# Kernel tuning notes

Measured on AMD Instinct MI355X. Metric: run time of the kernel, lower is better.

Reference implementation:

```python
import jax, jax.numpy as jnp
import numpy as np
from jax import lax

B, N, C = 8, 1024, 768
H, D = 12, 64
K = 3  # conv kernel size


def dwconv_over_batch(x, w, b):
    """Faithful port of SpatialDepthWisePerHeadConvolution as used in this module.
    x: [B, N, H, D]. The original code treats dim0 (B) as the conv length axis.
    w: [H*D, 1, K] depthwise kernel, b: [H*D].
    Returns [B, N, H, D].
    """
    b_, n_, h_, d_ = x.shape
    xc = jnp.transpose(x, (1, 2, 3, 0)).reshape(n_, h_ * d_, b_)  # [N, HD, B]
    y = lax.conv_general_dilated(
        xc, w, window_strides=(1,), padding=[(K - 1, K - 1)],
        feature_group_count=h_ * d_, dimension_numbers=("NCH", "OIH", "NCH"))
    y = y[:, :, :b_] + b[None, :, None]  # causal slice (drop last K-1)
    return jnp.transpose(y.reshape(n_, h_, d_, b_), (3, 0, 1, 2))


def setup_inputs() -> dict:
    key = jax.random.key(0)
    ks = jax.random.split(key, 12)
    s = 0.02
    inp = {
        "x": jax.random.normal(ks[0], (B, N, C), jnp.float32),
        "wq": jax.random.normal(ks[1], (C, H * D), jnp.float32) * s,
        "wk": jax.random.normal(ks[2], (C, H * D), jnp.float32) * s,
        "wv": jax.random.normal(ks[3], (C, H * D), jnp.float32) * s,
        "bv": jnp.zeros((H * D,), jnp.float32),
        "cq_w": jax.random.normal(ks[4], (H * D, 1, K), jnp.float32) * s,
        "cq_b": jnp.zeros((H * D,), jnp.float32),
        "ck_w": jax.random.normal(ks[5], (H * D, 1, K), jnp.float32) * s,
        "ck_b": jnp.zeros((H * D,), jnp.float32),
        "cv_w": jax.random.normal(ks[6], (H * D, 1, K), jnp.float32) * s,
        "cv_b": jnp.zeros((H * D,), jnp.float32),
        "wo": jax.random.normal(ks[7], (C, C), jnp.float32) * s,
        "bo": jnp.zeros((C,), jnp.float32),
    }
    return inp


def reference(x, wq, wk, wv, bv, cq_w, cq_b, ck_w, ck_b, cv_w, cv_b, wo, bo):
    scale = (C // H) ** -0.5
    # linear -> [B,N,H,D]
    q = (x @ wq).reshape(B, N, H, D)
    k = (x @ wk).reshape(B, N, H, D)
    v = ((x @ wv) + bv).reshape(B, N, H, D)
    # per-head depthwise causal conv (over batch axis, as in the original code)
    q = dwconv_over_batch(q, cq_w, cq_b)
    k = dwconv_over_batch(k, ck_w, ck_b)
    v = dwconv_over_batch(v, cv_w, cv_b)
    # [B,H,N,D]
    q = jnp.transpose(q, (0, 2, 1, 3))
    k = jnp.transpose(k, (0, 2, 1, 3))
    v = jnp.transpose(v, (0, 2, 1, 3))
    scores = jnp.einsum("bhnd,bhmd->bhnm", q, k) * scale
    attn = jax.nn.softmax(scores, axis=-1)
    out = jnp.einsum("bhnm,bhmd->bhnd", attn, v)
    out = jnp.transpose(out, (0, 2, 1, 3)).reshape(B, N, C)
    return out @ wo + bo
```

## Files before the change

kernel.cpp:

```cpp
#include <hip/hip_runtime.h>
#include <math.h>

static constexpr int B_ = 8, N_ = 1024, C_ = 768, H_ = 12, D_ = 64;

typedef __bf16 bf16_t;
typedef bf16_t bf16x8 __attribute__((ext_vector_type(8)));
typedef bf16_t bf16x4 __attribute__((ext_vector_type(4)));
typedef short short4v __attribute__((ext_vector_type(4)));
typedef float f32x4 __attribute__((ext_vector_type(4)));

#define MFMA32(a, b, c) __builtin_amdgcn_mfma_f32_16x16x32_bf16((a), (b), (c), 0, 0, 0)
#define MFMA16(a, b, c) __builtin_amdgcn_mfma_f32_16x16x16bf16_1k( \
    __builtin_bit_cast(short4v, (a)), __builtin_bit_cast(short4v, (b)), (c), 0, 0, 0)

__device__ __forceinline__ unsigned short f2bf(float f) {
    unsigned u = __builtin_bit_cast(unsigned, f);
    u += 0x7FFFu + ((u >> 16) & 1u);
    return (unsigned short)(u >> 16);
}

__device__ __forceinline__ float bf2f(unsigned short u) {
    return __builtin_bit_cast(float, (unsigned)u << 16);
}

__device__ __forceinline__ void gload16(void* lds, const void* g) {
    __builtin_amdgcn_global_load_lds(
        (const __attribute__((address_space(1))) unsigned int*)g,
        (__attribute__((address_space(3))) unsigned int*)lds, 16, 0, 0);
}

__device__ __forceinline__ int swz(int row, int kslot) {
    return row * 128 + (((kslot ^ row) & 7) << 4);
}

__global__ __launch_bounds__(256)
void castx_kernel(const float* __restrict__ in, unsigned short* __restrict__ out)
{
    const int i = blockIdx.x * 256 + threadIdx.x;
    const float4 a = ((const float4*)in)[2 * i];
    const float4 b = ((const float4*)in)[2 * i + 1];
    uint4 o;
    o.x = f2bf(a.x) | ((unsigned)f2bf(a.y) << 16);
    o.y = f2bf(a.z) | ((unsigned)f2bf(a.w) << 16);
    o.z = f2bf(b.x) | ((unsigned)f2bf(b.y) << 16);
    o.w = f2bf(b.z) | ((unsigned)f2bf(b.w) << 16);
    ((uint4*)out)[i] = o;
}

__global__ __launch_bounds__(256)
void castwT4_kernel(const float* w0, const float* w1, const float* w2, const float* w3,
                    unsigned short* o0, unsigned short* o1,
                    unsigned short* o2, unsigned short* o3)
{
    const float* w; unsigned short* wT;
    switch (blockIdx.z) {
        case 0:  w = w0; wT = o0; break;
        case 1:  w = w1; wT = o1; break;
        case 2:  w = w2; wT = o2; break;
        default: w = w3; wT = o3; break;
    }
    __shared__ float T[64][65];
    const int t = threadIdx.x;
    const int k0 = blockIdx.x * 64, n0 = blockIdx.y * 64;
    const int r = t >> 2, c0 = (t & 3) * 16;
#pragma unroll
    for (int j4 = 0; j4 < 4; ++j4) {
        const float4 v = *(const float4*)(w + (size_t)(k0 + r) * 768 + n0 + c0 + j4 * 4);
        T[r][c0 + j4 * 4 + 0] = v.x; T[r][c0 + j4 * 4 + 1] = v.y;
        T[r][c0 + j4 * 4 + 2] = v.z; T[r][c0 + j4 * 4 + 3] = v.w;
    }
    __syncthreads();
    const int nn = t >> 2;
    unsigned short o[16];
#pragma unroll
    for (int j = 0; j < 16; ++j) o[j] = f2bf(T[c0 + j][nn]);
    uint4* dst = (uint4*)(wT + (size_t)(n0 + nn) * 768 + k0 + c0);
    dst[0] = *(uint4*)(o); dst[1] = *(uint4*)(o + 8);
}

template <typename OutT>
__device__ __forceinline__ void gemm_body(const unsigned short* __restrict__ A,
                                          const unsigned short* __restrict__ BT,
                                          const float* __restrict__ bias,
                                          OutT* __restrict__ Cmat,
                                          int Ncols, int Kdim, int row0, int col0)
{
    __shared__ char As[128 * 128];
    __shared__ char Bs[128 * 128];

    const int tid = threadIdx.x, lane = tid & 63, w = tid >> 6;
    const int wr = w >> 1, wc = w & 1;
    const int slot = lane & 7, rsub = lane >> 3;

    f32x4 acc[4][4] = {};

    for (int k0 = 0; k0 < Kdim; k0 += 64) {
#pragma unroll
        for (int c = 0; c < 4; ++c) {
            const int chunk = c * 4 + w;
            const int r = chunk * 8 + rsub;
            gload16(As + chunk * 1024, A + (size_t)(row0 + r) * Kdim + k0 + 8 * (slot ^ (r & 7)));
            gload16(Bs + chunk * 1024, BT + (size_t)(col0 + r) * Kdim + k0 + 8 * (slot ^ (r & 7)));
        }
        __syncthreads();

#pragma unroll
        for (int kk = 0; kk < 2; ++kk) {
            const int kslot = kk * 4 + (lane >> 4);
            bf16x8 af[4], bf[4];
#pragma unroll
            for (int mi = 0; mi < 4; ++mi)
                af[mi] = *(const bf16x8*)(As + swz(wr * 64 + mi * 16 + (lane & 15), kslot));
#pragma unroll
            for (int ni = 0; ni < 4; ++ni)
                bf[ni] = *(const bf16x8*)(Bs + swz(wc * 64 + ni * 16 + (lane & 15), kslot));
#pragma unroll
            for (int mi = 0; mi < 4; ++mi)
#pragma unroll
                for (int ni = 0; ni < 4; ++ni)
                    acc[mi][ni] = MFMA32(af[mi], bf[ni], acc[mi][ni]);
        }
        __syncthreads();
    }

#pragma unroll
    for (int mi = 0; mi < 4; ++mi) {
        const int row = row0 + wr * 64 + mi * 16 + ((lane >> 4) << 2);
#pragma unroll
        for (int ni = 0; ni < 4; ++ni) {
            const int col = col0 + wc * 64 + ni * 16 + (lane & 15);
            const float bv_ = bias ? bias[col] : 0.f;
#pragma unroll
            for (int r = 0; r < 4; ++r) {
                const float v = acc[mi][ni][r] + bv_;
                if constexpr (sizeof(OutT) == 2)
                    Cmat[(size_t)(row + r) * Ncols + col] = (OutT)f2bf(v);
                else
                    Cmat[(size_t)(row + r) * Ncols + col] = v;
            }
        }
    }
}

__global__ __launch_bounds__(256)
void gemm_qkv(const unsigned short* __restrict__ xb,
              const unsigned short* __restrict__ wqT, const unsigned short* __restrict__ wkT,
              const unsigned short* __restrict__ wvT, const float* __restrict__ bv,
              unsigned short* __restrict__ q_lin, unsigned short* __restrict__ k_lin,
              unsigned short* __restrict__ v_lin)
{
    const int by = blockIdx.y, sel = by / 6, colt = by % 6;
    const unsigned short* BT; unsigned short* dst; const float* bias = nullptr;
    if (sel == 0)      { BT = wqT; dst = q_lin; }
    else if (sel == 1) { BT = wkT; dst = k_lin; }
    else               { BT = wvT; dst = v_lin; bias = bv; }
    gemm_body<unsigned short>(xb, BT, bias, dst, C_, C_, blockIdx.x * 128, colt * 128);
}

__global__ __launch_bounds__(256)
void gemm_proj(const unsigned short* __restrict__ A, const unsigned short* __restrict__ BT,
               const float* __restrict__ bias, float* __restrict__ Cmat)
{
    gemm_body<float>(A, BT, bias, Cmat, C_, C_, blockIdx.x * 128, blockIdx.y * 128);
}

__global__ __launch_bounds__(256)
void dwconv_qk(const unsigned short* __restrict__ qlin, const unsigned short* __restrict__ klin,
               const float* __restrict__ cq_w, const float* __restrict__ cq_b,
               const float* __restrict__ ck_w, const float* __restrict__ ck_b,
               unsigned short* __restrict__ qc, unsigned short* __restrict__ kc)
{
    const unsigned short* lin; const float* w; const float* bias;
    unsigned short* out;
    if (blockIdx.y == 0) { lin = qlin; w = cq_w; bias = cq_b; out = qc; }
    else                 { lin = klin; w = ck_w; bias = ck_b; out = kc; }

    const int i = blockIdx.x * 256 + threadIdx.x;
    const int c8 = i % (C_ / 8);
    const int n  = (i / (C_ / 8)) % N_;
    const int b  = i / ((C_ / 8) * N_);
    const int c  = c8 * 8;

    const uint4 z4 = make_uint4(0, 0, 0, 0);
    const uint4 x0 = (b >= 2) ? *(const uint4*)(lin + ((size_t)(b - 2) * N_ + n) * C_ + c) : z4;
    const uint4 x1 = (b >= 1) ? *(const uint4*)(lin + ((size_t)(b - 1) * N_ + n) * C_ + c) : z4;
    const uint4 x2 = *(const uint4*)(lin + ((size_t)b * N_ + n) * C_ + c);
    const unsigned short* u0 = (const unsigned short*)&x0;
    const unsigned short* u1 = (const unsigned short*)&x1;
    const unsigned short* u2 = (const unsigned short*)&x2;

    unsigned short y[8];
#pragma unroll
    for (int j = 0; j < 8; ++j) {
        const float v = w[(c + j) * 3 + 0] * bf2f(u0[j]) +
                        w[(c + j) * 3 + 1] * bf2f(u1[j]) +
                        w[(c + j) * 3 + 2] * bf2f(u2[j]) + bias[c + j];
        y[j] = f2bf(v);
    }
    const int h = c8 >> 3, d0 = (c8 & 7) * 8;
    *(uint4*)(out + (((size_t)b * H_ + h) * N_ + n) * 64 + d0) = *(uint4*)y;
}

__global__ __launch_bounds__(256)
void conv_v_transpose(const unsigned short* __restrict__ vlin, const float* __restrict__ w,
                      const float* __restrict__ bias, unsigned short* __restrict__ vt)
{
    __shared__ unsigned short T[64][72];
    const int t = threadIdx.x;
    const int n0 = blockIdx.x * 64, bh = blockIdx.y;
    const int b = bh / H_, h = bh % H_;
    const int r = t >> 2, c0 = (t & 3) * 16;
    const int cbase = h * 64 + c0;

    float acc[16];
#pragma unroll
    for (int i = 0; i < 16; ++i) acc[i] = bias[cbase + i];
#pragma unroll
    for (int j = 0; j < 3; ++j) {
        const int bb = b - 2 + j;
        if (bb < 0) continue;
        const unsigned short* src = vlin + ((size_t)bb * N_ + n0 + r) * C_ + cbase;
        const uint4 va = *(const uint4*)src;
        const uint4 vb2 = *(const uint4*)(src + 8);
        const unsigned short* u = (const unsigned short*)&va;
        const unsigned short* u2 = (const unsigned short*)&vb2;
#pragma unroll
        for (int i = 0; i < 8; ++i)  acc[i]     += w[(cbase + i) * 3 + j] * bf2f(u[i]);
#pragma unroll
        for (int i = 0; i < 8; ++i)  acc[8 + i] += w[(cbase + 8 + i) * 3 + j] * bf2f(u2[i]);
    }
    unsigned short tmp[16];
#pragma unroll
    for (int i = 0; i < 16; ++i) tmp[i] = f2bf(acc[i]);
    *(uint4*)&T[r][c0] = *(uint4*)tmp;
    *(uint4*)&T[r][c0 + 8] = *(uint4*)(tmp + 8);
    __syncthreads();

    const int d = t >> 2;
    unsigned short o[16];
#pragma unroll
    for (int i = 0; i < 16; ++i) o[i] = T[c0 + i][d];
    uint4* dst = (uint4*)(vt + ((size_t)bh * 64 + d) * N_ + n0 + c0);
    dst[0] = *(uint4*)o; dst[1] = *(uint4*)(o + 8);
}

__global__ __launch_bounds__(256)
void attn_mfma(const unsigned short* __restrict__ Qg, const unsigned short* __restrict__ Kg,
               const unsigned short* __restrict__ Vtg, unsigned short* __restrict__ Og)
{
    __shared__ char Kb[2][8192];
    __shared__ char Vb[2][8192];

    const int tid = threadIdx.x, lane = tid & 63, w = tid >> 6;
    const int g = lane >> 4, q = lane & 15;
    const int slot = lane & 7, rsub = lane >> 3;

    const int id = blockIdx.x;
    const int bh = (id & 7) * 12 + ((id >> 3) % 12);
    const int q0 = (id / 96) * 128;
    const int b = bh / H_, h = bh % H_;

    const unsigned short* Qp = Qg + (size_t)bh * N_ * 64;
    const unsigned short* Kp = Kg + (size_t)bh * N_ * 64;
    const unsigned short* Vp = Vtg + (size_t)bh * 64 * N_;

    bf16x8 qf[2][2];
#pragma unroll
    for (int mi = 0; mi < 2; ++mi)
#pragma unroll
        for (int kk = 0; kk < 2; ++kk)
            qf[mi][kk] = *(const bf16x8*)(Qp + (size_t)(q0 + w * 32 + mi * 16 + q) * 64 + kk * 32 + g * 8);

#pragma unroll
    for (int c = 0; c < 2; ++c) {
        const int chunk = c * 4 + w, r = chunk * 8 + rsub;
        gload16(Kb[0] + chunk * 1024, Kp + (size_t)r * 64 + 8 * (slot ^ (r & 7)));
        gload16(Vb[0] + chunk * 1024, Vp + (size_t)r * N_ + 8 * (slot ^ (r & 7)));
    }
    __syncthreads();

    f32x4 o[2][4] = {};
    float mrun[2] = {0.f, 0.f}, lrun[2] = {0.f, 0.f};
    const float cs = 0.18033688011112042f;

    int buf = 0;
    for (int kt = 0; kt < N_ / 64; ++kt) {
        if (kt < N_ / 64 - 1) {
            const int nb = buf ^ 1;
#pragma unroll
            for (int c = 0; c < 2; ++c) {
                const int chunk = c * 4 + w, r = chunk * 8 + rsub;
                gload16(Kb[nb] + chunk * 1024, Kp + (size_t)((kt + 1) * 64 + r) * 64 + 8 * (slot ^ (r & 7)));
                gload16(Vb[nb] + chunk * 1024, Vp + (size_t)r * N_ + (kt + 1) * 64 + 8 * (slot ^ (r & 7)));
            }
        }

        f32x4 s[2][4] = {};
#pragma unroll
        for (int kk = 0; kk < 2; ++kk) {
            const int kslot = kk * 4 + g;
            bf16x8 kf[4];
#pragma unroll
            for (int ni = 0; ni < 4; ++ni)
                kf[ni] = *(const bf16x8*)(Kb[buf] + swz(ni * 16 + q, kslot));
#pragma unroll
            for (int mi = 0; mi < 2; ++mi)
#pragma unroll
                for (int ni = 0; ni < 4; ++ni)
                    s[mi][ni] = MFMA32(kf[ni], qf[mi][kk], s[mi][ni]);
        }

        bf16x4 pf[2][4];
#pragma unroll
        for (int mi = 0; mi < 2; ++mi) {
            float t[4][4];
#pragma unroll
            for (int ni = 0; ni < 4; ++ni)
#pragma unroll
                for (int rg = 0; rg < 4; ++rg) t[ni][rg] = s[mi][ni][rg] * cs;
            float m0 = t[0][0];
#pragma unroll
            for (int ni = 0; ni < 4; ++ni)
#pragma unroll
                for (int rg = 0; rg < 4; ++rg) m0 = fmaxf(m0, t[ni][rg]);
            m0 = fmaxf(m0, __shfl_xor(m0, 16));
            m0 = fmaxf(m0, __shfl_xor(m0, 32));
            if (__any(m0 > mrun[mi] + 8.f)) {
                const float mnew = fmaxf(mrun[mi], m0);
                const float f = exp2f(mrun[mi] - mnew);
                lrun[mi] *= f;
#pragma unroll
                for (int nd = 0; nd < 4; ++nd) o[mi][nd] *= f;
                mrun[mi] = mnew;
            }
            float sum = 0.f;
#pragma unroll
            for (int ni = 0; ni < 4; ++ni) {
                const float p0 = exp2f(t[ni][0] - mrun[mi]);
                const float p1 = exp2f(t[ni][1] - mrun[mi]);
                const float p2 = exp2f(t[ni][2] - mrun[mi]);
                const float p3 = exp2f(t[ni][3] - mrun[mi]);
                sum += (p0 + p1) + (p2 + p3);
                bf16x4 pk;
                pk[0] = (bf16_t)p0; pk[1] = (bf16_t)p1; pk[2] = (bf16_t)p2; pk[3] = (bf16_t)p3;
                pf[mi][ni] = pk;
            }
            sum += __shfl_xor(sum, 16);
            sum += __shfl_xor(sum, 32);
            lrun[mi] += sum;
        }

#pragma unroll
        for (int ni = 0; ni < 4; ++ni) {
            bf16x4 vf[4];
#pragma unroll
            for (int nd = 0; nd < 4; ++nd) {
                const int d = nd * 16 + q;
                vf[nd] = *(const bf16x4*)(Vb[buf] + d * 128 +
                          ((((2 * ni + (g >> 1)) ^ (d & 7))) << 4) + 8 * (g & 1));
            }
#pragma unroll
            for (int mi = 0; mi < 2; ++mi)
#pragma unroll
                for (int nd = 0; nd < 4; ++nd)
                    o[mi][nd] = MFMA16(vf[nd], pf[mi][ni], o[mi][nd]);
        }

        __syncthreads();
        buf ^= 1;
    }

#pragma unroll
    for (int mi = 0; mi < 2; ++mi) {
        const float inv = 1.0f / lrun[mi];
        const int qrow = q0 + w * 32 + mi * 16 + q;
        unsigned short* orow = Og + ((size_t)b * N_ + qrow) * C_ + h * D_;
#pragma unroll
        for (int nd = 0; nd < 4; ++nd) {
            unsigned short pk[4];
#pragma unroll
            for (int rg = 0; rg < 4; ++rg) pk[rg] = f2bf(o[mi][nd][rg] * inv);
            *(uint2*)(orow + nd * 16 + 4 * g) = *(uint2*)pk;
        }
    }
}

extern "C" void kernel_launch(void* const* d_in, const int* in_sizes, int n_in,
                              void* d_out, int out_size, void* d_ws, size_t ws_size,
                              hipStream_t stream)
{
    (void)in_sizes; (void)n_in; (void)out_size; (void)ws_size;
    const float* x    = (const float*)d_in[0];
    const float* wq   = (const float*)d_in[1];
    const float* wk   = (const float*)d_in[2];
    const float* wv   = (const float*)d_in[3];
    const float* bv   = (const float*)d_in[4];
    const float* cq_w = (const float*)d_in[5];
    const float* cq_b = (const float*)d_in[6];
    const float* ck_w = (const float*)d_in[7];
    const float* ck_b = (const float*)d_in[8];
    const float* cv_w = (const float*)d_in[9];
    const float* cv_b = (const float*)d_in[10];
    const float* wo   = (const float*)d_in[11];
    const float* bo   = (const float*)d_in[12];
    float* out = (float*)d_out;

    char* wsb = (char*)d_ws;
    const size_t T  = (size_t)B_ * N_ * C_;
    const size_t WB = (size_t)2 * 589824;
    unsigned short* xb  = (unsigned short*)wsb;
    unsigned short* wqT = (unsigned short*)(wsb + 2 * T);
    unsigned short* wkT = wqT + 589824;
    unsigned short* wvT = wkT + 589824;
    unsigned short* woT = wvT + 589824;
    char* p = wsb + 2 * T + 4 * WB;
    unsigned short* q_lin = (unsigned short*)p;          p += 2 * T;
    unsigned short* k_lin = (unsigned short*)p;          p += 2 * T;
    unsigned short* v_lin = (unsigned short*)p;          p += 2 * T;
    unsigned short* qc    = (unsigned short*)p;          p += 2 * T;
    unsigned short* kc    = (unsigned short*)p;          p += 2 * T;
    unsigned short* vt    = (unsigned short*)p;          p += 2 * T;
    unsigned short* attn_out = xb;

    const int M = B_ * N_;

    castx_kernel<<<dim3((int)(T / 8 / 256)), 256, 0, stream>>>(x, xb);
    castwT4_kernel<<<dim3(12, 12, 4), 256, 0, stream>>>(wq, wk, wv, wo, wqT, wkT, wvT, woT);

    gemm_qkv<<<dim3(M / 128, 18), 256, 0, stream>>>(xb, wqT, wkT, wvT, bv, q_lin, k_lin, v_lin);

    dwconv_qk<<<dim3((int)(T / 8 / 256), 2), 256, 0, stream>>>(
        q_lin, k_lin, cq_w, cq_b, ck_w, ck_b, qc, kc);
    conv_v_transpose<<<dim3(N_ / 64, B_ * H_), 256, 0, stream>>>(v_lin, cv_w, cv_b, vt);

    attn_mfma<<<dim3(768), 256, 0, stream>>>(qc, kc, vt, attn_out);

    gemm_proj<<<dim3(M / 128, C_ / 128), 256, 0, stream>>>(attn_out, woT, bo, out);
}
```

Measured before the change: 277.8 us.

## Halve attention query tile to 64 rows per block, doubling grid size

```diff
diff --git a/kernel.cpp b/kernel.cpp
--- a/kernel.cpp
+++ b/kernel.cpp
@@ -257,19 +257,17 @@
 
     const int id = blockIdx.x;
     const int bh = (id & 7) * 12 + ((id >> 3) % 12);
-    const int q0 = (id / 96) * 128;
+    const int q0 = (id / 96) * 64;
     const int b = bh / H_, h = bh % H_;
 
     const unsigned short* Qp = Qg + (size_t)bh * N_ * 64;
     const unsigned short* Kp = Kg + (size_t)bh * N_ * 64;
     const unsigned short* Vp = Vtg + (size_t)bh * 64 * N_;
 
-    bf16x8 qf[2][2];
-#pragma unroll
-    for (int mi = 0; mi < 2; ++mi)
-#pragma unroll
-        for (int kk = 0; kk < 2; ++kk)
-            qf[mi][kk] = *(const bf16x8*)(Qp + (size_t)(q0 + w * 32 + mi * 16 + q) * 64 + kk * 32 + g * 8);
+    bf16x8 qf[2];
+#pragma unroll
+    for (int kk = 0; kk < 2; ++kk)
+        qf[kk] = *(const bf16x8*)(Qp + (size_t)(q0 + w * 16 + q) * 64 + kk * 32 + g * 8);
 
 #pragma unroll
     for (int c = 0; c < 2; ++c) {
@@ -279,8 +277,8 @@
     }
     __syncthreads();
 
-    f32x4 o[2][4] = {};
-    float mrun[2] = {0.f, 0.f}, lrun[2] = {0.f, 0.f};
+    f32x4 o[4] = {};
+    float mrun = 0.f, lrun = 0.f;
     const float cs = 0.18033688011112042f;
 
     int buf = 0;
@@ -295,7 +293,7 @@
             }
         }
 
-        f32x4 s[2][4] = {};
+        f32x4 s[4] = {};
 #pragma unroll
         for (int kk = 0; kk < 2; ++kk) {
             const int kslot = kk * 4 + g;
@@ -304,20 +302,17 @@
             for (int ni = 0; ni < 4; ++ni)
                 kf[ni] = *(const bf16x8*)(Kb[buf] + swz(ni * 16 + q, kslot));
 #pragma unroll
-            for (int mi = 0; mi < 2; ++mi)
-#pragma unroll
-                for (int ni = 0; ni < 4; ++ni)
-                    s[mi][ni] = MFMA32(kf[ni], qf[mi][kk], s[mi][ni]);
-        }
-
-        bf16x4 pf[2][4];
-#pragma unroll
-        for (int mi = 0; mi < 2; ++mi) {
+            for (int ni = 0; ni < 4; ++ni)
+                s[ni] = MFMA32(kf[ni], qf[kk], s[ni]);
+        }
+
+        bf16x4 pf[4];
+        {
             float t[4][4];
 #pragma unroll
             for (int ni = 0; ni < 4; ++ni)
 #pragma unroll
-                for (int rg = 0; rg < 4; ++rg) t[ni][rg] = s[mi][ni][rg] * cs;
+                for (int rg = 0; rg < 4; ++rg) t[ni][rg] = s[ni][rg] * cs;
             float m0 = t[0][0];
 #pragma unroll
             for (int ni = 0; ni < 4; ++ni)
@@ -325,29 +320,29 @@
                 for (int rg = 0; rg < 4; ++rg) m0 = fmaxf(m0, t[ni][rg]);
             m0 = fmaxf(m0, __shfl_xor(m0, 16));
             m0 = fmaxf(m0, __shfl_xor(m0, 32));
-            if (__any(m0 > mrun[mi] + 8.f)) {
-                const float mnew = fmaxf(mrun[mi], m0);
-                const float f = exp2f(mrun[mi] - mnew);
-                lrun[mi] *= f;
-#pragma unroll
-                for (int nd = 0; nd < 4; ++nd) o[mi][nd] *= f;
-                mrun[mi] = mnew;
+            if (__any(m0 > mrun + 8.f)) {
+                const float mnew = fmaxf(mrun, m0);
+                const float f = exp2f(mrun - mnew);
+                lrun *= f;
+#pragma unroll
+                for (int nd = 0; nd < 4; ++nd) o[nd] *= f;
+                mrun = mnew;
             }
             float sum = 0.f;
 #pragma unroll
             for (int ni = 0; ni < 4; ++ni) {
-                const float p0 = exp2f(t[ni][0] - mrun[mi]);
-                const float p1 = exp2f(t[ni][1] - mrun[mi]);
-                const float p2 = exp2f(t[ni][2] - mrun[mi]);
-                const float p3 = exp2f(t[ni][3] - mrun[mi]);
+                const float p0 = exp2f(t[ni][0] - mrun);
+                const float p1 = exp2f(t[ni][1] - mrun);
+                const float p2 = exp2f(t[ni][2] - mrun);
+                const float p3 = exp2f(t[ni][3] - mrun);
                 sum += (p0 + p1) + (p2 + p3);
                 bf16x4 pk;
                 pk[0] = (bf16_t)p0; pk[1] = (bf16_t)p1; pk[2] = (bf16_t)p2; pk[3] = (bf16_t)p3;
-                pf[mi][ni] = pk;
+                pf[ni] = pk;
             }
             sum += __shfl_xor(sum, 16);
             sum += __shfl_xor(sum, 32);
-            lrun[mi] += sum;
+            lrun += sum;
         }
 
 #pragma unroll
@@ -360,26 +355,23 @@
                           ((((2 * ni + (g >> 1)) ^ (d & 7))) << 4) + 8 * (g & 1));
             }
 #pragma unroll
-            for (int mi = 0; mi < 2; ++mi)
-#pragma unroll
-                for (int nd = 0; nd < 4; ++nd)
-                    o[mi][nd] = MFMA16(vf[nd], pf[mi][ni], o[mi][nd]);
+            for (int nd = 0; nd < 4; ++nd)
+                o[nd] = MFMA16(vf[nd], pf[ni], o[nd]);
         }
 
         __syncthreads();
         buf ^= 1;
     }
 
-#pragma unroll
-    for (int mi = 0; mi < 2; ++mi) {
-        const float inv = 1.0f / lrun[mi];
-        const int qrow = q0 + w * 32 + mi * 16 + q;
+    {
+        const float inv = 1.0f / lrun;
+        const int qrow = q0 + w * 16 + q;
         unsigned short* orow = Og + ((size_t)b * N_ + qrow) * C_ + h * D_;
 #pragma unroll
         for (int nd = 0; nd < 4; ++nd) {
             unsigned short pk[4];
 #pragma unroll
-            for (int rg = 0; rg < 4; ++rg) pk[rg] = f2bf(o[mi][nd][rg] * inv);
+            for (int rg = 0; rg < 4; ++rg) pk[rg] = f2bf(o[nd][rg] * inv);
             *(uint2*)(orow + nd * 16 + 4 * g) = *(uint2*)pk;
         }
     }
@@ -433,7 +425,7 @@
         q_lin, k_lin, cq_w, cq_b, ck_w, ck_b, qc, kc);
     conv_v_transpose<<<dim3(N_ / 64, B_ * H_), 256, 0, stream>>>(v_lin, cv_w, cv_b, vt);
 
-    attn_mfma<<<dim3(768), 256, 0, stream>>>(qc, kc, vt, attn_out);
+    attn_mfma<<<dim3(1536), 256, 0, stream>>>(qc, kc, vt, attn_out);
 
     gemm_proj<<<dim3(M / 128, C_ / 128), 256, 0, stream>>>(attn_out, woT, bo, out);
 }
```

New measurement: 275.7 us. About the same (-0.8%).
